# Kernel tuning notes

Measured on AMD Instinct MI355X. Metric: run time of the kernel, lower is better.

## Reference

```python
import jax, jax.numpy as jnp
import numpy as np

H = 128   # hidden_dim
L = 3     # num_layers
N = 50000
E = 800000
EPS = 1e-5


def setup_inputs() -> dict:
    key = jax.random.key(0)
    ks = jax.random.split(key, 16)
    s = 0.02  # param init scale
    return {
        "edge_index_new": jax.random.randint(ks[0], (2, E), 0, N),
        "aligned_features": jax.random.normal(ks[1], (E, 8), jnp.float32),
        "h_nodes_old": jax.random.normal(ks[2], (N, H), jnp.float32),
        "num_nodes": N,
        # node_fusion: Linear(2H -> H)
        "Wf": jax.random.normal(ks[3], (2 * H, H), jnp.float32) * s,
        "bf": jnp.zeros((H,), jnp.float32),
        # edge_to_weight: Linear(8->H), Linear(H->1)
        "We1": jax.random.normal(ks[4], (8, H), jnp.float32) * s,
        "be1": jnp.zeros((H,), jnp.float32),
        "We2": jax.random.normal(ks[5], (H, 1), jnp.float32) * s,
        "be2": jnp.zeros((1,), jnp.float32),
        # GraphConv per layer: lin_rel (W+b), lin_root (W, no bias)
        "Wrel": jax.random.normal(ks[6], (L, H, H), jnp.float32) * s,
        "brel": jnp.zeros((L, H), jnp.float32),
        "Wroot": jax.random.normal(ks[7], (L, H, H), jnp.float32) * s,
        # LayerNorm per layer
        "gamma": jnp.ones((L, H), jnp.float32),
        "beta": jnp.zeros((L, H), jnp.float32),
        # edge_decoder: Linear(2H+8 -> H), Linear(H -> 1)
        "Wd1": jax.random.normal(ks[8], (2 * H + 8, H), jnp.float32) * s,
        "bd1": jnp.zeros((H,), jnp.float32),
        "Wd2": jax.random.normal(ks[9], (H, 1), jnp.float32) * s,
        "bd2": jnp.zeros((1,), jnp.float32),
    }


def _layer_norm(x, g, b):
    mu = jnp.mean(x, axis=-1, keepdims=True)
    var = jnp.mean((x - mu) ** 2, axis=-1, keepdims=True)
    return (x - mu) * jax.lax.rsqrt(var + EPS) * g + b


def reference(edge_index_new, aligned_features, h_nodes_old, num_nodes,
              Wf, bf, We1, be1, We2, be2,
              Wrel, brel, Wroot, gamma, beta,
              Wd1, bd1, Wd2, bd2):
    dt = h_nodes_old.dtype
    hd = Wf.shape[1]
    # node_fusion(cat([ones, h_old])) ; dropout is identity in eval
    x_init = jnp.ones((num_nodes, hd), dtype=dt)
    x = jax.nn.relu(jnp.concatenate([x_init, h_nodes_old], axis=-1) @ Wf + bf)
    # edge_to_weight -> scalar per edge
    ew = jax.nn.sigmoid(jax.nn.relu(aligned_features @ We1 + be1) @ We2 + be2)[:, 0]
    src, dst = edge_index_new[0], edge_index_new[1]
    n_layers = Wrel.shape[0]
    for l in range(n_layers):
        x_res = x
        # GraphConv: sum_{j->i} w_e * x[j], then lin_rel(agg) + lin_root(x)
        msg = ew[:, None] * x[src]                         # [E, H]
        agg = jax.ops.segment_sum(msg, dst, num_segments=num_nodes)
        h = agg @ Wrel[l] + brel[l] + x @ Wroot[l]
        h = jax.nn.relu(_layer_norm(h, gamma[l], beta[l]))
        x = h + x_res
    # edge decoder on gathered node pairs + raw 8-dim features
    edge_repr = jnp.concatenate([x[src], x[dst], aligned_features], axis=-1)
    hmid = jax.nn.relu(edge_repr @ Wd1 + bd1)
    return hmid @ Wd2 + bd2
```

## Files before the change

### kernel.cpp

```cpp
#include <hip/hip_runtime.h>
#include <hip/hip_bf16.h>

#define H 128
#define LN_EPS 1e-5f

typedef __attribute__((ext_vector_type(8))) short bf16x8;
typedef __attribute__((ext_vector_type(4))) float f32x4;

static __device__ __forceinline__ unsigned short f2bf(float f) {
  unsigned u = __float_as_uint(f);
  unsigned r = (u + 0x7fff + ((u >> 16) & 1)) >> 16;
  return (unsigned short)r;
}
static __device__ __forceinline__ float bf2f(unsigned short s) {
  return __uint_as_float(((unsigned)s) << 16);
}


__global__ void zero_int_kernel(int* __restrict__ p, int n) {
  int i = blockIdx.x * blockDim.x + threadIdx.x;
  if (i < n) p[i] = 0;
}

__global__ __launch_bounds__(1024) void prep_cvec_kernel(const float* __restrict__ Wf,
                                                         const float* __restrict__ bf,
                                                         float* __restrict__ cvec) {
  __shared__ float part[8][128];
  int tid = threadIdx.x;
  int col = tid & 127, seg = tid >> 7;
  float s = 0.f;
  for (int r = seg * 16; r < seg * 16 + 16; ++r) s += Wf[r * H + col];
  part[seg][col] = s;
  __syncthreads();
  if (tid < 128) {
    float t = bf[tid];
#pragma unroll
    for (int g = 0; g < 8; ++g) t += part[g][tid];
    cvec[tid] = t;
  }
}

__global__ void count_kernel(const int* __restrict__ ei, int E, int* __restrict__ cnt) {
  int e = blockIdx.x * blockDim.x + threadIdx.x;
  if (e < E) atomicAdd(&cnt[ei[E + e]], 1);
}

__global__ __launch_bounds__(1024) void scan_kernel(const int* __restrict__ cnt,
                                                    int* __restrict__ off,
                                                    int* __restrict__ pos, int N) {
  __shared__ int wtot[16];
  __shared__ int wbase[16];
  __shared__ int s_btot;
  __shared__ int s_carry;
  int tid = threadIdx.x, lane = tid & 63, wid = tid >> 6;
  if (tid == 0) s_carry = 0;
  __syncthreads();
  for (int base = 0; base < N; base += 4096) {
    int i0 = base + tid * 4;
    int v[4];
#pragma unroll
    for (int j = 0; j < 4; ++j) v[j] = (i0 + j < N) ? cnt[i0 + j] : 0;
    int s = v[0] + v[1] + v[2] + v[3];
    int incl = s;
#pragma unroll
    for (int o = 1; o < 64; o <<= 1) {
      int t = __shfl_up(incl, o, 64);
      if (lane >= o) incl += t;
    }
    if (lane == 63) wtot[wid] = incl;
    __syncthreads();
    if (tid == 0) {
      int run = 0;
      for (int w = 0; w < 16; ++w) { wbase[w] = run; run += wtot[w]; }
      s_btot = run;
    }
    __syncthreads();
    int e0 = s_carry + wbase[wid] + (incl - s);
#pragma unroll
    for (int j = 0; j < 4; ++j) {
      if (i0 + j < N) { off[i0 + j] = e0; pos[i0 + j] = e0; }
      e0 += v[j];
    }
    __syncthreads();
    if (tid == 0) s_carry += s_btot;
    __syncthreads();
  }
  if (tid == 0) off[N] = s_carry;
}

__global__ __launch_bounds__(256) void pack_w_kernel(const float* __restrict__ Wf,
                                                     const float* __restrict__ Wrel,
                                                     const float* __restrict__ Wroot,
                                                     const float* __restrict__ Wd1,
                                                     unsigned short* __restrict__ wpk) {
  int id = blockIdx.x * blockDim.x + threadIdx.x;
  if (id >= 9 * 2048) return;
  int l = id & 63, nf = (id >> 6) & 7, kk = (id >> 9) & 3, m = id >> 11;
  const float* src;
  if (m == 0) src = Wf + H * H;
  else if (m <= 3) src = Wrel + (size_t)(m - 1) * H * H;
  else if (m <= 6) src = Wroot + (size_t)(m - 4) * H * H;
  else src = Wd1 + (size_t)(m - 7) * H * H;
  int col = nf * 16 + (l & 15);
  int kbase = kk * 32 + (l >> 4) * 8;
  unsigned short t[8];
#pragma unroll
  for (int j = 0; j < 8; ++j) t[j] = f2bf(src[(size_t)(kbase + j) * H + col]);
  *(uint4*)&wpk[(size_t)id * 8] = *(uint4*)t;
}

__global__ __launch_bounds__(256) void edge_weight_v3_kernel(
    const float* __restrict__ af, const float* __restrict__ We1, const float* __restrict__ be1,
    const float* __restrict__ We2, const float* __restrict__ be2, float* __restrict__ ew, int E) {
  int lane = threadIdx.x & 63;
  int sub = lane & 15;
  int grp = lane >> 4;
  float w1[8][8], b1[8], w2[8];
#pragma unroll
  for (int i = 0; i < 8; ++i)
#pragma unroll
    for (int c = 0; c < 8; ++c) w1[i][c] = We1[i * H + sub * 8 + c];
#pragma unroll
  for (int c = 0; c < 8; ++c) { b1[c] = be1[sub * 8 + c]; w2[c] = We2[sub * 8 + c]; }
  float b2 = be2[0];
  int gw = (blockIdx.x * blockDim.x + threadIdx.x) >> 6;
  int nw = (gridDim.x * blockDim.x) >> 6;
  int n4 = (E + 3) >> 2;
  for (int e4 = gw; e4 < n4; e4 += nw) {
    int e = e4 * 4 + grp;
    bool valid = e < E;
    int ee = valid ? e : E - 1;
    float4 a0 = *(const float4*)&af[(size_t)ee * 8];
    float4 a1 = *(const float4*)&af[(size_t)ee * 8 + 4];
    float afv[8] = {a0.x, a0.y, a0.z, a0.w, a1.x, a1.y, a1.z, a1.w};
    float t[8];
#pragma unroll
    for (int c = 0; c < 8; ++c) t[c] = b1[c];
#pragma unroll
    for (int i = 0; i < 8; ++i)
#pragma unroll
      for (int c = 0; c < 8; ++c) t[c] += afv[i] * w1[i][c];
    float p = 0.f;
#pragma unroll
    for (int c = 0; c < 8; ++c) p += fmaxf(t[c], 0.f) * w2[c];
    p += __shfl_xor(p, 1, 64);
    p += __shfl_xor(p, 2, 64);
    p += __shfl_xor(p, 4, 64);
    p += __shfl_xor(p, 8, 64);
    if (valid && sub == 0) {
      float s = p + b2;
      ew[e] = 1.f / (1.f + expf(-s));
    }
  }
}

__global__ void fill_v2_kernel(const int* __restrict__ ei, const float* __restrict__ ew, int E,
                               int* __restrict__ pos, uint4* __restrict__ csr4) {
  int e = blockIdx.x * blockDim.x + threadIdx.x;
  if (e < E) {
    int d = ei[E + e];
    int p = atomicAdd(&pos[d], 1);
    csr4[p] = make_uint4((unsigned)ei[e], __float_as_uint(ew[e]), (unsigned)e, (unsigned)d);
  }
}

__global__ __launch_bounds__(256) void gemm_init_kernel(
    const float* __restrict__ Xf, const unsigned short* __restrict__ Wp,
    const float* __restrict__ bias, unsigned short* __restrict__ Y, int M) {
  int l = threadIdx.x & 63, w = threadIdx.x >> 6;
  int lr = l & 15, lg = l >> 4;
  int m0 = blockIdx.x * 128 + w * 32;
  f32x4 acc[2][8] = {};
  for (int kk = 0; kk < 4; ++kk) {
    bf16x8 a[2];
#pragma unroll
    for (int mi = 0; mi < 2; ++mi) {
      int row = m0 + mi * 16 + lr;
      if (row >= M) row = M - 1;
      const float* xp = &Xf[(size_t)row * H + kk * 32 + lg * 8];
      float4 u0 = *(const float4*)xp;
      float4 u1 = *(const float4*)(xp + 4);
      unsigned short t[8] = {f2bf(u0.x), f2bf(u0.y), f2bf(u0.z), f2bf(u0.w),
                             f2bf(u1.x), f2bf(u1.y), f2bf(u1.z), f2bf(u1.w)};
      a[mi] = *(const bf16x8*)t;
    }
#pragma unroll
    for (int nf = 0; nf < 8; ++nf) {
      bf16x8 b = *(const bf16x8*)&Wp[(size_t)(kk * 8 + nf) * 512 + l * 8];
#pragma unroll
      for (int mi = 0; mi < 2; ++mi)
        acc[mi][nf] = __builtin_amdgcn_mfma_f32_16x16x32_bf16(a[mi], b, acc[mi][nf], 0, 0, 0);
    }
  }
  float bv[8];
#pragma unroll
  for (int nf = 0; nf < 8; ++nf) bv[nf] = bias[nf * 16 + lr];
#pragma unroll
  for (int mi = 0; mi < 2; ++mi)
#pragma unroll
    for (int r = 0; r < 4; ++r) {
      int row = m0 + mi * 16 + lg * 4 + r;
      if (row < M) {
#pragma unroll
        for (int nf = 0; nf < 8; ++nf)
          Y[(size_t)row * H + nf * 16 + lr] = f2bf(fmaxf(acc[mi][nf][r] + bv[nf], 0.f));
      }
    }
}

__global__ __launch_bounds__(256) void gemm_layer_ln_kernel(
    const unsigned short* __restrict__ Agg, const unsigned short* __restrict__ WpRel,
    unsigned short* __restrict__ Xio, const unsigned short* __restrict__ WpRoot,
    const float* __restrict__ brel, const float* __restrict__ gamma,
    const float* __restrict__ beta, int M) {
  int l = threadIdx.x & 63, w = threadIdx.x >> 6;
  int lr = l & 15, lg = l >> 4;
  int m0 = blockIdx.x * 128 + w * 32;
  f32x4 acc[2][8] = {};
  for (int kk = 0; kk < 8; ++kk) {
    const unsigned short* X = (kk >= 4) ? Xio : Agg;
    const unsigned short* Wp = (kk >= 4) ? WpRoot : WpRel;
    int k4 = kk & 3;
    bf16x8 a[2] = {};
#pragma unroll
    for (int mi = 0; mi < 2; ++mi) {
      int row = m0 + mi * 16 + lr;
      if (row < M) a[mi] = *(const bf16x8*)&X[(size_t)row * H + k4 * 32 + lg * 8];
    }
#pragma unroll
    for (int nf = 0; nf < 8; ++nf) {
      bf16x8 b = *(const bf16x8*)&Wp[(size_t)(k4 * 8 + nf) * 512 + l * 8];
#pragma unroll
      for (int mi = 0; mi < 2; ++mi)
        acc[mi][nf] = __builtin_amdgcn_mfma_f32_16x16x32_bf16(a[mi], b, acc[mi][nf], 0, 0, 0);
    }
  }
  float bv[8], gv[8], bev[8];
#pragma unroll
  for (int nf = 0; nf < 8; ++nf) {
    int col = nf * 16 + lr;
    bv[nf] = brel[col]; gv[nf] = gamma[col]; bev[nf] = beta[col];
  }
#pragma unroll
  for (int mi = 0; mi < 2; ++mi) {
#pragma unroll
    for (int r = 0; r < 4; ++r) {
      int row = m0 + mi * 16 + lg * 4 + r;
      float hv[8], s1 = 0.f;
#pragma unroll
      for (int nf = 0; nf < 8; ++nf) { hv[nf] = acc[mi][nf][r] + bv[nf]; s1 += hv[nf]; }
      s1 += __shfl_xor(s1, 1, 64);
      s1 += __shfl_xor(s1, 2, 64);
      s1 += __shfl_xor(s1, 4, 64);
      s1 += __shfl_xor(s1, 8, 64);
      float mu = s1 * (1.0f / H);
      float s2 = 0.f;
#pragma unroll
      for (int nf = 0; nf < 8; ++nf) { float d = hv[nf] - mu; s2 += d * d; }
      s2 += __shfl_xor(s2, 1, 64);
      s2 += __shfl_xor(s2, 2, 64);
      s2 += __shfl_xor(s2, 4, 64);
      s2 += __shfl_xor(s2, 8, 64);
      float rstd = rsqrtf(s2 * (1.0f / H) + LN_EPS);
      if (row < M) {
#pragma unroll
        for (int nf = 0; nf < 8; ++nf) {
          int col = nf * 16 + lr;
          float v = fmaxf((hv[nf] - mu) * rstd * gv[nf] + bev[nf], 0.f);
          v += bf2f(Xio[(size_t)row * H + col]);
          Xio[(size_t)row * H + col] = f2bf(v);
        }
      }
    }
  }
}

__global__ __launch_bounds__(256) void gemm_dec_kernel(
    const unsigned short* __restrict__ X, const unsigned short* __restrict__ WpA,
    const unsigned short* __restrict__ WpB, const float* __restrict__ bd1,
    unsigned short* __restrict__ Aout, unsigned short* __restrict__ Bout, int M) {
  int l = threadIdx.x & 63, w = threadIdx.x >> 6;
  int lr = l & 15, lg = l >> 4;
  int m0 = blockIdx.x * 128 + w * 32;
  f32x4 accA[2][8] = {};
  f32x4 accB[2][8] = {};
  for (int kk = 0; kk < 4; ++kk) {
    bf16x8 a[2];
#pragma unroll
    for (int mi = 0; mi < 2; ++mi) {
      int row = m0 + mi * 16 + lr;
      if (row >= M) row = M - 1;
      a[mi] = *(const bf16x8*)&X[(size_t)row * H + kk * 32 + lg * 8];
    }
#pragma unroll
    for (int nf = 0; nf < 8; ++nf) {
      bf16x8 bA = *(const bf16x8*)&WpA[(size_t)(kk * 8 + nf) * 512 + l * 8];
      bf16x8 bB = *(const bf16x8*)&WpB[(size_t)(kk * 8 + nf) * 512 + l * 8];
#pragma unroll
      for (int mi = 0; mi < 2; ++mi) {
        accA[mi][nf] = __builtin_amdgcn_mfma_f32_16x16x32_bf16(a[mi], bA, accA[mi][nf], 0, 0, 0);
        accB[mi][nf] = __builtin_amdgcn_mfma_f32_16x16x32_bf16(a[mi], bB, accB[mi][nf], 0, 0, 0);
      }
    }
  }
  float bdv[8];
#pragma unroll
  for (int nf = 0; nf < 8; ++nf) bdv[nf] = bd1[nf * 16 + lr];
#pragma unroll
  for (int mi = 0; mi < 2; ++mi)
#pragma unroll
    for (int r = 0; r < 4; ++r) {
      int row = m0 + mi * 16 + lg * 4 + r;
      if (row < M) {
#pragma unroll
        for (int nf = 0; nf < 8; ++nf) {
          int col = nf * 16 + lr;
          Aout[(size_t)row * H + col] = f2bf(accA[mi][nf][r] + bdv[nf]);
          Bout[(size_t)row * H + col] = f2bf(accB[mi][nf][r]);
        }
      }
    }
}

__global__ __launch_bounds__(256) void gather_agg_v4_kernel(
    const unsigned short* __restrict__ xbf, const int* __restrict__ off,
    const uint4* __restrict__ csr4, unsigned short* __restrict__ aggbf, int N) {
  int gw = (blockIdx.x * blockDim.x + threadIdx.x) >> 6;
  int lane = threadIdx.x & 63;
  int q = lane >> 4, li = lane & 15;
  int n = gw * 4 + q;
  if (n >= N) return;
  int s0 = off[n], s1 = off[n + 1];
  float a0 = 0.f, a1 = 0.f, a2 = 0.f, a3 = 0.f, a4 = 0.f, a5 = 0.f, a6 = 0.f, a7 = 0.f;
  for (int base = s0; base < s1; base += 16) {
    uint2 c[16];
#pragma unroll
    for (int j = 0; j < 16; ++j) {
      int id = base + j;
      c[j] = *(const uint2*)&csr4[id < s1 ? id : s1 - 1];
      if (id >= s1) c[j].y = 0;
    }
    uint4 v[16];
#pragma unroll
    for (int j = 0; j < 16; ++j)
      v[j] = *(const uint4*)&xbf[(size_t)c[j].x * H + li * 8];
#pragma unroll
    for (int j = 0; j < 16; ++j) {
      float w = __uint_as_float(c[j].y);
      a0 += w * bf2f((unsigned short)(v[j].x & 0xffffu));
      a1 += w * bf2f((unsigned short)(v[j].x >> 16));
      a2 += w * bf2f((unsigned short)(v[j].y & 0xffffu));
      a3 += w * bf2f((unsigned short)(v[j].y >> 16));
      a4 += w * bf2f((unsigned short)(v[j].z & 0xffffu));
      a5 += w * bf2f((unsigned short)(v[j].z >> 16));
      a6 += w * bf2f((unsigned short)(v[j].w & 0xffffu));
      a7 += w * bf2f((unsigned short)(v[j].w >> 16));
    }
  }
  unsigned short t[8] = {f2bf(a0), f2bf(a1), f2bf(a2), f2bf(a3),
                         f2bf(a4), f2bf(a5), f2bf(a6), f2bf(a7)};
  *(uint4*)&aggbf[(size_t)n * H + li * 8] = *(uint4*)t;
}

__global__ __launch_bounds__(256) void edge_out_v6_kernel(
    const uint4* __restrict__ csr4, const float* __restrict__ af,
    const unsigned short* __restrict__ A, const unsigned short* __restrict__ B,
    const float* __restrict__ Wd1c, const float* __restrict__ Wd2,
    const float* __restrict__ bd2, float* __restrict__ out, int E) {
  int lane = threadIdx.x & 63;
  int sub = lane & 15;
  int grp = lane >> 4;
  float wc[8][8], w2[8];
#pragma unroll
  for (int i = 0; i < 8; ++i)
#pragma unroll
    for (int c = 0; c < 8; ++c) wc[i][c] = Wd1c[i * H + sub * 8 + c];
#pragma unroll
  for (int c = 0; c < 8; ++c) w2[c] = Wd2[sub * 8 + c];
  float b2 = bd2[0];
  int gw = (blockIdx.x * blockDim.x + threadIdx.x) >> 6;
  int nw = (gridDim.x * blockDim.x) >> 6;
  int n4 = (E + 3) >> 2;
  for (int e4 = gw; e4 < n4; e4 += nw) {
    int idx = e4 * 4 + grp;
    bool valid = idx < E;
    int ii = valid ? idx : E - 1;
    uint4 c = csr4[ii];
    uint4 va = *(const uint4*)&A[(size_t)c.x * H + sub * 8];
    uint4 vb = *(const uint4*)&B[(size_t)c.w * H + sub * 8];
    float4 f0 = *(const float4*)&af[(size_t)c.z * 8];
    float4 f1 = *(const float4*)&af[(size_t)c.z * 8 + 4];
    const unsigned* pa = (const unsigned*)&va;
    const unsigned* pb = (const unsigned*)&vb;
    float t[8];
#pragma unroll
    for (int q = 0; q < 4; ++q) {
      t[q * 2 + 0] = bf2f((unsigned short)(pa[q] & 0xffffu)) + bf2f((unsigned short)(pb[q] & 0xffffu));
      t[q * 2 + 1] = bf2f((unsigned short)(pa[q] >> 16)) + bf2f((unsigned short)(pb[q] >> 16));
    }
    float afv[8] = {f0.x, f0.y, f0.z, f0.w, f1.x, f1.y, f1.z, f1.w};
#pragma unroll
    for (int i = 0; i < 8; ++i)
#pragma unroll
      for (int cc = 0; cc < 8; ++cc) t[cc] += afv[i] * wc[i][cc];
    float p = 0.f;
#pragma unroll
    for (int cc = 0; cc < 8; ++cc) p += fmaxf(t[cc], 0.f) * w2[cc];
    p += __shfl_xor(p, 1, 64);
    p += __shfl_xor(p, 2, 64);
    p += __shfl_xor(p, 4, 64);
    p += __shfl_xor(p, 8, 64);
    if (valid && sub == 0) out[c.z] = p + b2;
  }
}

extern "C" void kernel_launch(void* const* d_in, const int* in_sizes, int n_in, void* d_out,
                              int out_size, void* d_ws, size_t ws_size, hipStream_t stream) {
  const int* ei = (const int*)d_in[0];
  const float* af = (const float*)d_in[1];
  const float* h_old = (const float*)d_in[2];
  const float* Wf = (const float*)d_in[4];
  const float* bf = (const float*)d_in[5];
  const float* We1 = (const float*)d_in[6];
  const float* be1 = (const float*)d_in[7];
  const float* We2 = (const float*)d_in[8];
  const float* be2 = (const float*)d_in[9];
  const float* Wrel = (const float*)d_in[10];
  const float* brel = (const float*)d_in[11];
  const float* Wroot = (const float*)d_in[12];
  const float* gamma = (const float*)d_in[13];
  const float* beta = (const float*)d_in[14];
  const float* Wd1 = (const float*)d_in[15];
  const float* bd1 = (const float*)d_in[16];
  const float* Wd2 = (const float*)d_in[17];
  const float* bd2 = (const float*)d_in[18];
  const int N = in_sizes[2] / H;
  const int E = in_sizes[1] / 8;
  float* out = (float*)d_out;

  char* p = (char*)d_ws;
  auto alloc = [&](size_t b) { char* r = p; p += (b + 255) & ~(size_t)255; return r; };
  int* cnt = (int*)alloc((size_t)N * 4);
  int* pos = (int*)alloc((size_t)N * 4);
  int* off = (int*)alloc((size_t)(N + 1) * 4);
  uint4* csr4 = (uint4*)alloc((size_t)E * 16);
  float* ew = (float*)alloc((size_t)E * 4);
  float* cvec = (float*)alloc(H * 4);
  unsigned short* wpk = (unsigned short*)alloc((size_t)9 * 16384 * 2);
  unsigned short* xbf = (unsigned short*)alloc((size_t)N * H * 2);
  unsigned short* aggbf = (unsigned short*)alloc((size_t)N * H * 2);
  unsigned short* buf2 = (unsigned short*)alloc((size_t)N * H * 2);

  unsigned short* Abf = aggbf;
  unsigned short* Bbf = buf2;

  hipLaunchKernelGGL(zero_int_kernel, dim3((N + 255) / 256), dim3(256), 0, stream, cnt, N);
  hipLaunchKernelGGL(prep_cvec_kernel, dim3(1), dim3(1024), 0, stream, Wf, bf, cvec);
  hipLaunchKernelGGL(count_kernel, dim3((E + 255) / 256), dim3(256), 0, stream, ei, E, cnt);
  hipLaunchKernelGGL(scan_kernel, dim3(1), dim3(1024), 0, stream, cnt, off, pos, N);
  hipLaunchKernelGGL(edge_weight_v3_kernel, dim3(4096), dim3(256), 0, stream, af, We1, be1,
                     We2, be2, ew, E);
  hipLaunchKernelGGL(fill_v2_kernel, dim3((E + 255) / 256), dim3(256), 0, stream, ei, ew, E,
                     pos, csr4);
  hipLaunchKernelGGL(pack_w_kernel, dim3(72), dim3(256), 0, stream, Wf, Wrel, Wroot, Wd1, wpk);

  int gblocks = (N + 127) / 128;
  hipLaunchKernelGGL(gemm_init_kernel, dim3(gblocks), dim3(256), 0, stream, h_old, wpk, cvec,
                     xbf, N);

  int gat4_blocks = (N + 15) / 16;
  for (int l = 0; l < 3; ++l) {
    hipLaunchKernelGGL(gather_agg_v4_kernel, dim3(gat4_blocks), dim3(256), 0, stream, xbf, off,
                       csr4, aggbf, N);
    hipLaunchKernelGGL(gemm_layer_ln_kernel, dim3(gblocks), dim3(256), 0, stream, aggbf,
                       wpk + (size_t)(1 + l) * 16384, xbf, wpk + (size_t)(4 + l) * 16384,
                       brel + l * H, gamma + l * H, beta + l * H, N);
  }

  hipLaunchKernelGGL(gemm_dec_kernel, dim3(gblocks), dim3(256), 0, stream, xbf,
                     wpk + (size_t)7 * 16384, wpk + (size_t)8 * 16384, bd1, Abf, Bbf, N);
  hipLaunchKernelGGL(edge_out_v6_kernel, dim3(4096), dim3(256), 0, stream, csr4, af, Abf, Bbf,
                     Wd1 + 2 * H * H, Wd2, bd2, out, E);
}
```

Measured before the change: 443.9 us.

## Merge preprocessing kernels into two multi-role launches to cut launch count

Edge-weight MLP, degree counting, cvec reduction and weight packing are merged into one heterogeneous kernel that dispatches on block index. The init GEMM and the CSR prefix scan are merged into a second kernel, with the scan now using a single 256-thread block. The zeroing kernel is replaced by hipMemsetAsync. This reduces launches and lets independent work overlap, at the cost of a slower single-block scan that may end up on the critical path.

```diff
diff --git a/kernel.cpp b/kernel.cpp
--- a/kernel.cpp
+++ b/kernel.cpp
@@ -3,6 +3,7 @@
 
 #define H 128
 #define LN_EPS 1e-5f
+#define EW_BLOCKS 4096
 
 typedef __attribute__((ext_vector_type(8))) short bf16x8;
 typedef __attribute__((ext_vector_type(4))) float f32x4;
@@ -16,141 +17,172 @@
   return __uint_as_float(((unsigned)s) << 16);
 }
 
-
-__global__ void zero_int_kernel(int* __restrict__ p, int n) {
-  int i = blockIdx.x * blockDim.x + threadIdx.x;
-  if (i < n) p[i] = 0;
-}
-
-__global__ __launch_bounds__(1024) void prep_cvec_kernel(const float* __restrict__ Wf,
-                                                         const float* __restrict__ bf,
-                                                         float* __restrict__ cvec) {
-  __shared__ float part[8][128];
+__global__ __launch_bounds__(256) void pre1_kernel(
+    const int* __restrict__ ei, const float* __restrict__ af, const float* __restrict__ We1,
+    const float* __restrict__ be1, const float* __restrict__ We2, const float* __restrict__ be2,
+    float* __restrict__ ew, int* __restrict__ cnt, const float* __restrict__ Wf,
+    const float* __restrict__ bf, float* __restrict__ cvec, const float* __restrict__ Wrel,
+    const float* __restrict__ Wroot, const float* __restrict__ Wd1,
+    unsigned short* __restrict__ wpk, int E, int cntBlocks) {
+  int b = blockIdx.x;
   int tid = threadIdx.x;
-  int col = tid & 127, seg = tid >> 7;
-  float s = 0.f;
-  for (int r = seg * 16; r < seg * 16 + 16; ++r) s += Wf[r * H + col];
-  part[seg][col] = s;
-  __syncthreads();
-  if (tid < 128) {
-    float t = bf[tid];
-#pragma unroll
-    for (int g = 0; g < 8; ++g) t += part[g][tid];
-    cvec[tid] = t;
-  }
-}
-
-__global__ void count_kernel(const int* __restrict__ ei, int E, int* __restrict__ cnt) {
-  int e = blockIdx.x * blockDim.x + threadIdx.x;
-  if (e < E) atomicAdd(&cnt[ei[E + e]], 1);
-}
-
-__global__ __launch_bounds__(1024) void scan_kernel(const int* __restrict__ cnt,
-                                                    int* __restrict__ off,
-                                                    int* __restrict__ pos, int N) {
-  __shared__ int wtot[16];
-  __shared__ int wbase[16];
-  __shared__ int s_btot;
-  __shared__ int s_carry;
-  int tid = threadIdx.x, lane = tid & 63, wid = tid >> 6;
-  if (tid == 0) s_carry = 0;
-  __syncthreads();
-  for (int base = 0; base < N; base += 4096) {
-    int i0 = base + tid * 4;
-    int v[4];
-#pragma unroll
-    for (int j = 0; j < 4; ++j) v[j] = (i0 + j < N) ? cnt[i0 + j] : 0;
-    int s = v[0] + v[1] + v[2] + v[3];
-    int incl = s;
-#pragma unroll
-    for (int o = 1; o < 64; o <<= 1) {
-      int t = __shfl_up(incl, o, 64);
-      if (lane >= o) incl += t;
-    }
-    if (lane == 63) wtot[wid] = incl;
+  if (b < EW_BLOCKS) {
+    int lane = tid & 63;
+    int sub = lane & 15;
+    int grp = lane >> 4;
+    float w1[8][8], b1[8], w2[8];
+#pragma unroll
+    for (int i = 0; i < 8; ++i)
+#pragma unroll
+      for (int c = 0; c < 8; ++c) w1[i][c] = We1[i * H + sub * 8 + c];
+#pragma unroll
+    for (int c = 0; c < 8; ++c) { b1[c] = be1[sub * 8 + c]; w2[c] = We2[sub * 8 + c]; }
+    float b2 = be2[0];
+    int gw = b * 4 + (tid >> 6);
+    int nw = EW_BLOCKS * 4;
+    int n4 = (E + 3) >> 2;
+    for (int e4 = gw; e4 < n4; e4 += nw) {
+      int e = e4 * 4 + grp;
+      bool valid = e < E;
+      int ee = valid ? e : E - 1;
+      float4 a0 = *(const float4*)&af[(size_t)ee * 8];
+      float4 a1 = *(const float4*)&af[(size_t)ee * 8 + 4];
+      float afv[8] = {a0.x, a0.y, a0.z, a0.w, a1.x, a1.y, a1.z, a1.w};
+      float t[8];
+#pragma unroll
+      for (int c = 0; c < 8; ++c) t[c] = b1[c];
+#pragma unroll
+      for (int i = 0; i < 8; ++i)
+#pragma unroll
+        for (int c = 0; c < 8; ++c) t[c] += afv[i] * w1[i][c];
+      float p = 0.f;
+#pragma unroll
+      for (int c = 0; c < 8; ++c) p += fmaxf(t[c], 0.f) * w2[c];
+      p += __shfl_xor(p, 1, 64);
+      p += __shfl_xor(p, 2, 64);
+      p += __shfl_xor(p, 4, 64);
+      p += __shfl_xor(p, 8, 64);
+      if (valid && sub == 0) {
+        float s = p + b2;
+        ew[e] = 1.f / (1.f + expf(-s));
+      }
+    }
+  } else if (b < EW_BLOCKS + cntBlocks) {
+    int e = (b - EW_BLOCKS) * 256 + tid;
+    if (e < E) atomicAdd(&cnt[ei[E + e]], 1);
+  } else if (b == EW_BLOCKS + cntBlocks) {
+    __shared__ float part[2][128];
+    int col = tid & 127, seg = tid >> 7;
+    float s = 0.f;
+    for (int r = seg * 64; r < seg * 64 + 64; ++r) s += Wf[r * H + col];
+    part[seg][col] = s;
     __syncthreads();
-    if (tid == 0) {
-      int run = 0;
-      for (int w = 0; w < 16; ++w) { wbase[w] = run; run += wtot[w]; }
-      s_btot = run;
-    }
+    if (tid < 128) cvec[tid] = bf[tid] + part[0][tid] + part[1][tid];
+  } else {
+    int id = (b - (EW_BLOCKS + cntBlocks + 1)) * 256 + tid;
+    if (id >= 9 * 2048) return;
+    int l = id & 63, nf = (id >> 6) & 7, kk = (id >> 9) & 3, m = id >> 11;
+    const float* src;
+    if (m == 0) src = Wf + H * H;
+    else if (m <= 3) src = Wrel + (size_t)(m - 1) * H * H;
+    else if (m <= 6) src = Wroot + (size_t)(m - 4) * H * H;
+    else src = Wd1 + (size_t)(m - 7) * H * H;
+    int col = nf * 16 + (l & 15);
+    int kbase = kk * 32 + (l >> 4) * 8;
+    unsigned short t[8];
+#pragma unroll
+    for (int j = 0; j < 8; ++j) t[j] = f2bf(src[(size_t)(kbase + j) * H + col]);
+    *(uint4*)&wpk[(size_t)id * 8] = *(uint4*)t;
+  }
+}
+
+__global__ __launch_bounds__(256) void pre2_kernel(
+    const float* __restrict__ Xf, const unsigned short* __restrict__ Wp,
+    const float* __restrict__ cvec, unsigned short* __restrict__ Y,
+    const int* __restrict__ cnt, int* __restrict__ off, int* __restrict__ pos, int M,
+    int gblocks) {
+  int b = blockIdx.x;
+  int tid = threadIdx.x;
+  if (b < gblocks) {
+    int l = tid & 63, w = tid >> 6;
+    int lr = l & 15, lg = l >> 4;
+    int m0 = b * 128 + w * 32;
+    f32x4 acc[2][8] = {};
+    for (int kk = 0; kk < 4; ++kk) {
+      bf16x8 a[2];
+#pragma unroll
+      for (int mi = 0; mi < 2; ++mi) {
+        int row = m0 + mi * 16 + lr;
+        if (row >= M) row = M - 1;
+        const float* xp = &Xf[(size_t)row * H + kk * 32 + lg * 8];
+        float4 u0 = *(const float4*)xp;
+        float4 u1 = *(const float4*)(xp + 4);
+        unsigned short t[8] = {f2bf(u0.x), f2bf(u0.y), f2bf(u0.z), f2bf(u0.w),
+                               f2bf(u1.x), f2bf(u1.y), f2bf(u1.z), f2bf(u1.w)};
+        a[mi] = *(const bf16x8*)t;
+      }
+#pragma unroll
+      for (int nf = 0; nf < 8; ++nf) {
+        bf16x8 bb = *(const bf16x8*)&Wp[(size_t)(kk * 8 + nf) * 512 + l * 8];
+#pragma unroll
+        for (int mi = 0; mi < 2; ++mi)
+          acc[mi][nf] = __builtin_amdgcn_mfma_f32_16x16x32_bf16(a[mi], bb, acc[mi][nf], 0, 0, 0);
+      }
+    }
+    float bv[8];
+#pragma unroll
+    for (int nf = 0; nf < 8; ++nf) bv[nf] = cvec[nf * 16 + lr];
+#pragma unroll
+    for (int mi = 0; mi < 2; ++mi)
+#pragma unroll
+      for (int r = 0; r < 4; ++r) {
+        int row = m0 + mi * 16 + lg * 4 + r;
+        if (row < M) {
+#pragma unroll
+          for (int nf = 0; nf < 8; ++nf)
+            Y[(size_t)row * H + nf * 16 + lr] = f2bf(fmaxf(acc[mi][nf][r] + bv[nf], 0.f));
+        }
+      }
+  } else {
+    __shared__ int wtot[4];
+    __shared__ int wbase[4];
+    __shared__ int s_btot;
+    __shared__ int s_carry;
+    int N = M;
+    int lane = tid & 63, wid = tid >> 6;
+    if (tid == 0) s_carry = 0;
     __syncthreads();
-    int e0 = s_carry + wbase[wid] + (incl - s);
-#pragma unroll
-    for (int j = 0; j < 4; ++j) {
-      if (i0 + j < N) { off[i0 + j] = e0; pos[i0 + j] = e0; }
-      e0 += v[j];
-    }
-    __syncthreads();
-    if (tid == 0) s_carry += s_btot;
-    __syncthreads();
-  }
-  if (tid == 0) off[N] = s_carry;
-}
-
-__global__ __launch_bounds__(256) void pack_w_kernel(const float* __restrict__ Wf,
-                                                     const float* __restrict__ Wrel,
-                                                     const float* __restrict__ Wroot,
-                                                     const float* __restrict__ Wd1,
-                                                     unsigned short* __restrict__ wpk) {
-  int id = blockIdx.x * blockDim.x + threadIdx.x;
-  if (id >= 9 * 2048) return;
-  int l = id & 63, nf = (id >> 6) & 7, kk = (id >> 9) & 3, m = id >> 11;
-  const float* src;
-  if (m == 0) src = Wf + H * H;
-  else if (m <= 3) src = Wrel + (size_t)(m - 1) * H * H;
-  else if (m <= 6) src = Wroot + (size_t)(m - 4) * H * H;
-  else src = Wd1 + (size_t)(m - 7) * H * H;
-  int col = nf * 16 + (l & 15);
-  int kbase = kk * 32 + (l >> 4) * 8;
-  unsigned short t[8];
-#pragma unroll
-  for (int j = 0; j < 8; ++j) t[j] = f2bf(src[(size_t)(kbase + j) * H + col]);
-  *(uint4*)&wpk[(size_t)id * 8] = *(uint4*)t;
-}
-
-__global__ __launch_bounds__(256) void edge_weight_v3_kernel(
-    const float* __restrict__ af, const float* __restrict__ We1, const float* __restrict__ be1,
-    const float* __restrict__ We2, const float* __restrict__ be2, float* __restrict__ ew, int E) {
-  int lane = threadIdx.x & 63;
-  int sub = lane & 15;
-  int grp = lane >> 4;
-  float w1[8][8], b1[8], w2[8];
-#pragma unroll
-  for (int i = 0; i < 8; ++i)
-#pragma unroll
-    for (int c = 0; c < 8; ++c) w1[i][c] = We1[i * H + sub * 8 + c];
-#pragma unroll
-  for (int c = 0; c < 8; ++c) { b1[c] = be1[sub * 8 + c]; w2[c] = We2[sub * 8 + c]; }
-  float b2 = be2[0];
-  int gw = (blockIdx.x * blockDim.x + threadIdx.x) >> 6;
-  int nw = (gridDim.x * blockDim.x) >> 6;
-  int n4 = (E + 3) >> 2;
-  for (int e4 = gw; e4 < n4; e4 += nw) {
-    int e = e4 * 4 + grp;
-    bool valid = e < E;
-    int ee = valid ? e : E - 1;
-    float4 a0 = *(const float4*)&af[(size_t)ee * 8];
-    float4 a1 = *(const float4*)&af[(size_t)ee * 8 + 4];
-    float afv[8] = {a0.x, a0.y, a0.z, a0.w, a1.x, a1.y, a1.z, a1.w};
-    float t[8];
-#pragma unroll
-    for (int c = 0; c < 8; ++c) t[c] = b1[c];
-#pragma unroll
-    for (int i = 0; i < 8; ++i)
-#pragma unroll
-      for (int c = 0; c < 8; ++c) t[c] += afv[i] * w1[i][c];
-    float p = 0.f;
-#pragma unroll
-    for (int c = 0; c < 8; ++c) p += fmaxf(t[c], 0.f) * w2[c];
-    p += __shfl_xor(p, 1, 64);
-    p += __shfl_xor(p, 2, 64);
-    p += __shfl_xor(p, 4, 64);
-    p += __shfl_xor(p, 8, 64);
-    if (valid && sub == 0) {
-      float s = p + b2;
-      ew[e] = 1.f / (1.f + expf(-s));
-    }
+    for (int base = 0; base < N; base += 1024) {
+      int i0 = base + tid * 4;
+      int v[4];
+#pragma unroll
+      for (int j = 0; j < 4; ++j) v[j] = (i0 + j < N) ? cnt[i0 + j] : 0;
+      int s = v[0] + v[1] + v[2] + v[3];
+      int incl = s;
+#pragma unroll
+      for (int o = 1; o < 64; o <<= 1) {
+        int t = __shfl_up(incl, o, 64);
+        if (lane >= o) incl += t;
+      }
+      if (lane == 63) wtot[wid] = incl;
+      __syncthreads();
+      if (tid == 0) {
+        int run = 0;
+        for (int w = 0; w < 4; ++w) { wbase[w] = run; run += wtot[w]; }
+        s_btot = run;
+      }
+      __syncthreads();
+      int e0 = s_carry + wbase[wid] + (incl - s);
+#pragma unroll
+      for (int j = 0; j < 4; ++j) {
+        if (i0 + j < N) { off[i0 + j] = e0; pos[i0 + j] = e0; }
+        e0 += v[j];
+      }
+      __syncthreads();
+      if (tid == 0) s_carry += s_btot;
+      __syncthreads();
+    }
+    if (tid == 0) off[N] = s_carry;
   }
 }
 
@@ -162,50 +194,6 @@
     int p = atomicAdd(&pos[d], 1);
     csr4[p] = make_uint4((unsigned)ei[e], __float_as_uint(ew[e]), (unsigned)e, (unsigned)d);
   }
-}
-
-__global__ __launch_bounds__(256) void gemm_init_kernel(
-    const float* __restrict__ Xf, const unsigned short* __restrict__ Wp,
-    const float* __restrict__ bias, unsigned short* __restrict__ Y, int M) {
-  int l = threadIdx.x & 63, w = threadIdx.x >> 6;
-  int lr = l & 15, lg = l >> 4;
-  int m0 = blockIdx.x * 128 + w * 32;
-  f32x4 acc[2][8] = {};
-  for (int kk = 0; kk < 4; ++kk) {
-    bf16x8 a[2];
-#pragma unroll
-    for (int mi = 0; mi < 2; ++mi) {
-      int row = m0 + mi * 16 + lr;
-      if (row >= M) row = M - 1;
-      const float* xp = &Xf[(size_t)row * H + kk * 32 + lg * 8];
-      float4 u0 = *(const float4*)xp;
-      float4 u1 = *(const float4*)(xp + 4);
-      unsigned short t[8] = {f2bf(u0.x), f2bf(u0.y), f2bf(u0.z), f2bf(u0.w),
-                             f2bf(u1.x), f2bf(u1.y), f2bf(u1.z), f2bf(u1.w)};
-      a[mi] = *(const bf16x8*)t;
-    }
-#pragma unroll
-    for (int nf = 0; nf < 8; ++nf) {
-      bf16x8 b = *(const bf16x8*)&Wp[(size_t)(kk * 8 + nf) * 512 + l * 8];
-#pragma unroll
-      for (int mi = 0; mi < 2; ++mi)
-        acc[mi][nf] = __builtin_amdgcn_mfma_f32_16x16x32_bf16(a[mi], b, acc[mi][nf], 0, 0, 0);
-    }
-  }
-  float bv[8];
-#pragma unroll
-  for (int nf = 0; nf < 8; ++nf) bv[nf] = bias[nf * 16 + lr];
-#pragma unroll
-  for (int mi = 0; mi < 2; ++mi)
-#pragma unroll
-    for (int r = 0; r < 4; ++r) {
-      int row = m0 + mi * 16 + lg * 4 + r;
-      if (row < M) {
-#pragma unroll
-        for (int nf = 0; nf < 8; ++nf)
-          Y[(size_t)row * H + nf * 16 + lr] = f2bf(fmaxf(acc[mi][nf][r] + bv[nf], 0.f));
-      }
-    }
 }
 
 __global__ __launch_bounds__(256) void gemm_layer_ln_kernel(
@@ -454,19 +442,17 @@
   unsigned short* Abf = aggbf;
   unsigned short* Bbf = buf2;
 
-  hipLaunchKernelGGL(zero_int_kernel, dim3((N + 255) / 256), dim3(256), 0, stream, cnt, N);
-  hipLaunchKernelGGL(prep_cvec_kernel, dim3(1), dim3(1024), 0, stream, Wf, bf, cvec);
-  hipLaunchKernelGGL(count_kernel, dim3((E + 255) / 256), dim3(256), 0, stream, ei, E, cnt);
-  hipLaunchKernelGGL(scan_kernel, dim3(1), dim3(1024), 0, stream, cnt, off, pos, N);
-  hipLaunchKernelGGL(edge_weight_v3_kernel, dim3(4096), dim3(256), 0, stream, af, We1, be1,
-                     We2, be2, ew, E);
-  hipLaunchKernelGGL(fill_v2_kernel, dim3((E + 255) / 256), dim3(256), 0, stream, ei, ew, E,
-                     pos, csr4);
-  hipLaunchKernelGGL(pack_w_kernel, dim3(72), dim3(256), 0, stream, Wf, Wrel, Wroot, Wd1, wpk);
-
+  int cntBlocks = (E + 255) / 256;
   int gblocks = (N + 127) / 128;
-  hipLaunchKernelGGL(gemm_init_kernel, dim3(gblocks), dim3(256), 0, stream, h_old, wpk, cvec,
-                     xbf, N);
+
+  hipMemsetAsync(cnt, 0, (size_t)N * 4, stream);
+  hipLaunchKernelGGL(pre1_kernel, dim3(EW_BLOCKS + cntBlocks + 1 + 72), dim3(256), 0, stream,
+                     ei, af, We1, be1, We2, be2, ew, cnt, Wf, bf, cvec, Wrel, Wroot, Wd1, wpk,
+                     E, cntBlocks);
+  hipLaunchKernelGGL(pre2_kernel, dim3(gblocks + 1), dim3(256), 0, stream, h_old, wpk, cvec,
+                     xbf, cnt, off, pos, N, gblocks);
+  hipLaunchKernelGGL(fill_v2_kernel, dim3(cntBlocks), dim3(256), 0, stream, ei, ew, E, pos,
+                     csr4);
 
   int gat4_blocks = (N + 15) / 16;
   for (int l = 0; l < 3; ++l) {
```

Result: no change. 438.8 us (-1.2%).
